# Kernel optimization log

Hardware: AMD Instinct MI355X
Metric: run time of the kernel (lower is better)

## Reference

```python
import jax, jax.numpy as jnp
import numpy as np

N_NODES = 1_000_000   # graph.number_of_nodes()
EMBED_D = 128         # config.embed_dim
WALK_L  = 100         # config.walk_len
WIN_K   = 5           # config.k_neighbor
N_NEG   = 5           # config.neg_sampling_per_pos
B_WALKS = 256         # batch of random walks


def _pair_offsets():
    # (i, j) index pairs within a walk: j in [i-k, i+k], j != i
    ci, cj = [], []
    for i in range(WALK_L):
        for j in range(max(0, i - WIN_K), min(i + WIN_K + 1, WALK_L)):
            if i != j:
                ci.append(i); cj.append(j)
    return np.asarray(ci), np.asarray(cj)


def setup_inputs() -> dict:
    key = jax.random.key(0)
    k1, k2, k3 = jax.random.split(key, 3)
    emb = jax.random.normal(k1, (N_NODES, EMBED_D), dtype=jnp.float32) * 0.1
    walks = np.asarray(jax.random.randint(k2, (B_WALKS, WALK_L), 0, N_NODES))
    ci, cj = _pair_offsets()
    centers = jnp.asarray(walks[:, ci].reshape(-1).astype(np.int32))   # [P]
    contexts = jnp.asarray(walks[:, cj].reshape(-1).astype(np.int32))  # [P]
    P = centers.shape[0]  # 248320
    negs = jax.random.randint(k3, (P, N_NEG), 0, N_NODES, dtype=jnp.int32)
    return {"emb": emb, "centers": centers, "contexts": contexts, "negs": negs}


def reference(emb, centers, contexts, negs):
    # Batched SGNS: gather + dot + logsigmoid over all (center, context, negs) triples.
    x_v = emb[centers]               # [P, D]
    x_c = emb[contexts]              # [P, D]
    x_n = emb[negs]                  # [P, NEG, D]
    pos_loss = -jax.nn.log_sigmoid(jnp.sum(x_v * x_c, axis=-1))                 # [P]
    neg_scores = jnp.einsum('pd,pkd->pk', -x_v, x_n)                            # [P, NEG]
    neg_loss = -jnp.sum(jax.nn.log_sigmoid(neg_scores), axis=-1)                # [P]
    return jnp.mean(pos_loss + neg_loss)  # total_loss / n
```

## Files before the change

### kernel.cpp

```cpp
#include <hip/hip_runtime.h>

constexpr int D   = 128;
constexpr int NEG = 5;

__device__ __forceinline__ float softplus_fast(float z) {
    float t = __builtin_amdgcn_exp2f(-fabsf(z) * 1.44269504f);
    return fmaxf(z, 0.0f) + 0.69314718f * __builtin_amdgcn_logf(1.0f + t);
}

__global__ void __launch_bounds__(256, 8)
sgns_loss_kernel(const float* __restrict__ emb,
                 const int*   __restrict__ centers,
                 const int*   __restrict__ contexts,
                 const int*   __restrict__ negs,
                 float* __restrict__ out,
                 int P, float invP) {
    __shared__ float bsum;
    if (threadIdx.x == 0) bsum = 0.0f;
    __syncthreads();

    const int lane = threadIdx.x & 63;
    const int sub  = lane & 31;
    const int gid  = (int)((blockIdx.x * blockDim.x + threadIdx.x) >> 5);
    const int ngrp = (int)((gridDim.x * blockDim.x) >> 5);

    float local = 0.0f;

    int p = gid;
    int ic = 0, io = 0, i0 = 0, i1 = 0, i2 = 0, i3 = 0, i4 = 0;
    if (p < P) {
        ic = centers[p];  io = contexts[p];
        const int* nb = negs + (size_t)p * NEG;
        i0 = nb[0]; i1 = nb[1]; i2 = nb[2]; i3 = nb[3]; i4 = nb[4];
    }

    while (p < P) {
        const float4 v  = ((const float4*)(emb + (size_t)ic * D))[sub];
        const float4 c  = ((const float4*)(emb + (size_t)io * D))[sub];
        const float4 n0 = ((const float4*)(emb + (size_t)i0 * D))[sub];
        const float4 n1 = ((const float4*)(emb + (size_t)i1 * D))[sub];
        const float4 n2 = ((const float4*)(emb + (size_t)i2 * D))[sub];
        const float4 n3 = ((const float4*)(emb + (size_t)i3 * D))[sub];
        const float4 n4 = ((const float4*)(emb + (size_t)i4 * D))[sub];

        const int pn = p + ngrp;
        if (pn < P) {
            ic = centers[pn];  io = contexts[pn];
            const int* nb = negs + (size_t)pn * NEG;
            i0 = nb[0]; i1 = nb[1]; i2 = nb[2]; i3 = nb[3]; i4 = nb[4];
        }

        float a0 = v.x*c.x  + v.y*c.y  + v.z*c.z  + v.w*c.w;
        float a1 = v.x*n0.x + v.y*n0.y + v.z*n0.z + v.w*n0.w;
        float a2 = v.x*n1.x + v.y*n1.y + v.z*n1.z + v.w*n1.w;
        float a3 = v.x*n2.x + v.y*n2.y + v.z*n2.z + v.w*n2.w;
        float a4 = v.x*n3.x + v.y*n3.y + v.z*n3.z + v.w*n3.w;
        float a5 = v.x*n4.x + v.y*n4.y + v.z*n4.z + v.w*n4.w;

#pragma unroll
        for (int off = 1; off < 32; off <<= 1) {
            a0 += __shfl_xor(a0, off, 64);
            a1 += __shfl_xor(a1, off, 64);
            a2 += __shfl_xor(a2, off, 64);
            a3 += __shfl_xor(a3, off, 64);
            a4 += __shfl_xor(a4, off, 64);
            a5 += __shfl_xor(a5, off, 64);
        }

        float loss = softplus_fast(-a0);
        loss += softplus_fast(a1);
        loss += softplus_fast(a2);
        loss += softplus_fast(a3);
        loss += softplus_fast(a4);
        loss += softplus_fast(a5);
        if (sub == 0) local += loss;

        p = pn;
    }

#pragma unroll
    for (int off = 1; off < 64; off <<= 1)
        local += __shfl_xor(local, off, 64);
    if (lane == 0 && local != 0.0f) atomicAdd(&bsum, local * invP);
    __syncthreads();
    if (threadIdx.x == 0) atomicAdd(out, bsum);
}

extern "C" void kernel_launch(void* const* d_in, const int* in_sizes, int n_in,
                              void* d_out, int out_size, void* d_ws, size_t ws_size,
                              hipStream_t stream) {
    const float* emb      = (const float*)d_in[0];
    const int*   centers  = (const int*)d_in[1];
    const int*   contexts = (const int*)d_in[2];
    const int*   negs     = (const int*)d_in[3];
    float*       out      = (float*)d_out;

    const int P = in_sizes[1];
    const float invP = 1.0f / (float)P;

    hipMemsetAsync(d_out, 0, sizeof(float) * out_size, stream);

    const int block = 256;
    const int grid  = 2048;
    sgns_loss_kernel<<<grid, block, 0, stream>>>(emb, centers, contexts, negs,
                                                 out, P, invP);
}
```

Measured before the change: 121.7 us.

## Use 8-lane groups per pair, one pair per group, and binned two-stage reduction

Each pair is now handled by an 8-thread group that loops over 4 chunks of the 128-d rows, instead of a 32-lane group over a grid-stride loop with index prefetch. The grid is sized to cover all pairs directly, giving many short-lived blocks. The final sum goes through 1024 padded bins with per-block atomics and then a separate single-block reduction kernel, replacing the single global atomic. This is meant to cut shuffle-reduction steps, raise memory-level parallelism and avoid contention on one atomic, at the cost of an extra kernel launch and the loss of the software index prefetch.

```diff
diff --git a/kernel.cpp b/kernel.cpp
--- a/kernel.cpp
+++ b/kernel.cpp
@@ -1,64 +1,63 @@
 #include <hip/hip_runtime.h>
 
-constexpr int D   = 128;
-constexpr int NEG = 5;
+constexpr int D         = 128;
+constexpr int NEG       = 5;
+constexpr int GSIZE     = 8;
+constexpr int CHUNKS    = D / (4 * GSIZE);
+constexpr int NBINS     = 1024;
+constexpr int BINSTRIDE = 16;
 
 __device__ __forceinline__ float softplus_fast(float z) {
     float t = __builtin_amdgcn_exp2f(-fabsf(z) * 1.44269504f);
     return fmaxf(z, 0.0f) + 0.69314718f * __builtin_amdgcn_logf(1.0f + t);
 }
 
-__global__ void __launch_bounds__(256, 8)
-sgns_loss_kernel(const float* __restrict__ emb,
+__global__ void __launch_bounds__(256)
+sgns_pair_kernel(const float* __restrict__ emb,
                  const int*   __restrict__ centers,
                  const int*   __restrict__ contexts,
                  const int*   __restrict__ negs,
-                 float* __restrict__ out,
+                 float* __restrict__ bins,
                  int P, float invP) {
-    __shared__ float bsum;
-    if (threadIdx.x == 0) bsum = 0.0f;
-    __syncthreads();
+    const int sub = threadIdx.x & (GSIZE - 1);
+    const int p   = blockIdx.x * (256 / GSIZE) + (threadIdx.x >> 3);
 
-    const int lane = threadIdx.x & 63;
-    const int sub  = lane & 31;
-    const int gid  = (int)((blockIdx.x * blockDim.x + threadIdx.x) >> 5);
-    const int ngrp = (int)((gridDim.x * blockDim.x) >> 5);
+    float contrib = 0.0f;
+    if (p < P) {
+        const int  ic = centers[p];
+        const int  io = contexts[p];
+        const int* nb = negs + (size_t)p * NEG;
+        const int  i0 = nb[0], i1 = nb[1], i2 = nb[2], i3 = nb[3], i4 = nb[4];
 
-    float local = 0.0f;
+        const float4* vr  = (const float4*)(emb + (size_t)ic * D);
+        const float4* cr  = (const float4*)(emb + (size_t)io * D);
+        const float4* nr0 = (const float4*)(emb + (size_t)i0 * D);
+        const float4* nr1 = (const float4*)(emb + (size_t)i1 * D);
+        const float4* nr2 = (const float4*)(emb + (size_t)i2 * D);
+        const float4* nr3 = (const float4*)(emb + (size_t)i3 * D);
+        const float4* nr4 = (const float4*)(emb + (size_t)i4 * D);
 
-    int p = gid;
-    int ic = 0, io = 0, i0 = 0, i1 = 0, i2 = 0, i3 = 0, i4 = 0;
-    if (p < P) {
-        ic = centers[p];  io = contexts[p];
-        const int* nb = negs + (size_t)p * NEG;
-        i0 = nb[0]; i1 = nb[1]; i2 = nb[2]; i3 = nb[3]; i4 = nb[4];
-    }
-
-    while (p < P) {
-        const float4 v  = ((const float4*)(emb + (size_t)ic * D))[sub];
-        const float4 c  = ((const float4*)(emb + (size_t)io * D))[sub];
-        const float4 n0 = ((const float4*)(emb + (size_t)i0 * D))[sub];
-        const float4 n1 = ((const float4*)(emb + (size_t)i1 * D))[sub];
-        const float4 n2 = ((const float4*)(emb + (size_t)i2 * D))[sub];
-        const float4 n3 = ((const float4*)(emb + (size_t)i3 * D))[sub];
-        const float4 n4 = ((const float4*)(emb + (size_t)i4 * D))[sub];
-
-        const int pn = p + ngrp;
-        if (pn < P) {
-            ic = centers[pn];  io = contexts[pn];
-            const int* nb = negs + (size_t)pn * NEG;
-            i0 = nb[0]; i1 = nb[1]; i2 = nb[2]; i3 = nb[3]; i4 = nb[4];
+        float a0 = 0.f, a1 = 0.f, a2 = 0.f, a3 = 0.f, a4 = 0.f, a5 = 0.f;
+#pragma unroll
+        for (int c = 0; c < CHUNKS; ++c) {
+            const int idx = sub + GSIZE * c;
+            const float4 v  = vr[idx];
+            const float4 cc = cr[idx];
+            const float4 n0 = nr0[idx];
+            const float4 n1 = nr1[idx];
+            const float4 n2 = nr2[idx];
+            const float4 n3 = nr3[idx];
+            const float4 n4 = nr4[idx];
+            a0 += v.x*cc.x + v.y*cc.y + v.z*cc.z + v.w*cc.w;
+            a1 += v.x*n0.x + v.y*n0.y + v.z*n0.z + v.w*n0.w;
+            a2 += v.x*n1.x + v.y*n1.y + v.z*n1.z + v.w*n1.w;
+            a3 += v.x*n2.x + v.y*n2.y + v.z*n2.z + v.w*n2.w;
+            a4 += v.x*n3.x + v.y*n3.y + v.z*n3.z + v.w*n3.w;
+            a5 += v.x*n4.x + v.y*n4.y + v.z*n4.z + v.w*n4.w;
         }
 
-        float a0 = v.x*c.x  + v.y*c.y  + v.z*c.z  + v.w*c.w;
-        float a1 = v.x*n0.x + v.y*n0.y + v.z*n0.z + v.w*n0.w;
-        float a2 = v.x*n1.x + v.y*n1.y + v.z*n1.z + v.w*n1.w;
-        float a3 = v.x*n2.x + v.y*n2.y + v.z*n2.z + v.w*n2.w;
-        float a4 = v.x*n3.x + v.y*n3.y + v.z*n3.z + v.w*n3.w;
-        float a5 = v.x*n4.x + v.y*n4.y + v.z*n4.z + v.w*n4.w;
-
 #pragma unroll
-        for (int off = 1; off < 32; off <<= 1) {
+        for (int off = 1; off < GSIZE; off <<= 1) {
             a0 += __shfl_xor(a0, off, 64);
             a1 += __shfl_xor(a1, off, 64);
             a2 += __shfl_xor(a2, off, 64);
@@ -73,17 +72,34 @@
         loss += softplus_fast(a3);
         loss += softplus_fast(a4);
         loss += softplus_fast(a5);
-        if (sub == 0) local += loss;
-
-        p = pn;
+        if (sub == 0) contrib = loss * invP;
     }
 
 #pragma unroll
+    for (int off = GSIZE; off < 64; off <<= 1)
+        contrib += __shfl_xor(contrib, off, 64);
+
+    __shared__ float bsum;
+    if (threadIdx.x == 0) bsum = 0.0f;
+    __syncthreads();
+    if ((threadIdx.x & 63) == 0) atomicAdd(&bsum, contrib);
+    __syncthreads();
+    if (threadIdx.x == 0)
+        atomicAdd(&bins[(blockIdx.x & (NBINS - 1)) * BINSTRIDE], bsum);
+}
+
+__global__ void __launch_bounds__(256)
+reduce_bins_kernel(const float* __restrict__ bins, float* __restrict__ out) {
+    float s = 0.0f;
+    for (int i = threadIdx.x; i < NBINS; i += 256)
+        s += bins[i * BINSTRIDE];
+#pragma unroll
     for (int off = 1; off < 64; off <<= 1)
-        local += __shfl_xor(local, off, 64);
-    if (lane == 0 && local != 0.0f) atomicAdd(&bsum, local * invP);
+        s += __shfl_xor(s, off, 64);
+    __shared__ float ws[4];
+    if ((threadIdx.x & 63) == 0) ws[threadIdx.x >> 6] = s;
     __syncthreads();
-    if (threadIdx.x == 0) atomicAdd(out, bsum);
+    if (threadIdx.x == 0) out[0] = ws[0] + ws[1] + ws[2] + ws[3];
 }
 
 extern "C" void kernel_launch(void* const* d_in, const int* in_sizes, int n_in,
@@ -93,15 +109,17 @@
     const int*   centers  = (const int*)d_in[1];
     const int*   contexts = (const int*)d_in[2];
     const int*   negs     = (const int*)d_in[3];
+    float*       bins     = (float*)d_ws;
     float*       out      = (float*)d_out;
 
     const int P = in_sizes[1];
     const float invP = 1.0f / (float)P;
 
-    hipMemsetAsync(d_out, 0, sizeof(float) * out_size, stream);
+    hipMemsetAsync(d_ws, 0, NBINS * BINSTRIDE * sizeof(float), stream);
 
     const int block = 256;
-    const int grid  = 2048;
-    sgns_loss_kernel<<<grid, block, 0, stream>>>(emb, centers, contexts, negs,
-                                                 out, P, invP);
+    const int grid  = (P + 31) / 32;
+    sgns_pair_kernel<<<grid, block, 0, stream>>>(emb, centers, contexts, negs,
+                                                 bins, P, invP);
+    reduce_bins_kernel<<<1, 256, 0, stream>>>(bins, out);
 }
```

Measured after the change: 106.9 us. 1.14x faster.
